# Performance work log

Hardware: AMD Instinct MI355X
Metric: run time of the kernel (lower is better)

## Reference

```python
import jax, jax.numpy as jnp
import numpy as np

B, L = 512, 8192          # batch, document length
N = 128                   # output_sentence_num
S = 256                   # output_sentence_len
DELIM = 5                 # delimiter token
PAD = 0                   # pad_word
CUT_HEAD = False
VOCAB = 100


def setup_inputs() -> dict:
    key = jax.random.key(0)
    x = jax.random.randint(key, (B, L), 0, VOCAB, dtype=jnp.int32)
    return {"x": x}


def reference(x):
    b, l = x.shape
    # right-padded row: original tokens + one trailing delimiter, shape [B, L+1]
    rpad = jnp.concatenate([x, jnp.full((b, 1), DELIM, x.dtype)], axis=1)
    # segment id of rpad position j = number of delimiters in x[:j]
    cum = jnp.cumsum((x == DELIM).astype(jnp.int32), axis=1)           # [B, L]
    seg = jnp.concatenate([jnp.zeros((b, 1), jnp.int32), cum], axis=1)  # [B, L+1]
    seg = jnp.minimum(seg, N - 1)  # segments >= N-1 merged into last chunk (tail merge)
    j = jnp.arange(l + 1, dtype=jnp.int32)
    bidx = jnp.arange(b)[:, None]
    # start index of each segment (min j with seg==k); unused segments stay at L+1
    starts = jnp.full((b, N), l + 1, jnp.int32)
    starts = starts.at[bidx, seg].min(jnp.broadcast_to(j, (b, l + 1)))
    pos = j[None, :] - jnp.take_along_axis(starts, seg, axis=1)  # offset within chunk
    # chunk sizes (number of rpad positions per segment)
    sizes = jnp.zeros((b, N), jnp.int32).at[bidx, seg].add(jnp.ones((b, l + 1), jnp.int32))
    size_here = jnp.take_along_axis(sizes, seg, axis=1)
    # size-1 chunks (lone delimiter == empty sentence) are filled with pad_word
    vals = jnp.where(size_here == 1, jnp.int32(PAD), rpad)
    if CUT_HEAD:
        p = pos - 1
        valid = (pos >= 1) & (pos <= S - 1)  # chunk[1:S], then padded to S
    else:
        p = pos
        valid = pos <= S - 1                 # chunk[:S]
    # scatter into [B, N, S]; invalid positions routed out-of-bounds and dropped
    k_idx = jnp.where(valid, seg, N)
    p_idx = jnp.where(valid, p, S)
    otp = jnp.full((b, N, S), PAD, x.dtype)
    otp = otp.at[bidx, k_idx, p_idx].set(vals, mode='drop')
    # lengths / mask (tf.count_nonzero semantics; pad_word == 0)
    len_sent = jnp.sum((otp != 0).astype(jnp.int32), axis=2)   # [B, N]
    len_doc = jnp.sum((len_sent != 0).astype(jnp.int32), axis=1)  # [B]
    mask = (jnp.arange(S)[None, None, :] < len_sent[..., None]).astype(jnp.float32)
    return otp, len_doc, mask
```

## Files before the change

### kernel.cpp

```cpp
#include <hip/hip_runtime.h>

#define B_ 512
#define L_ 8192
#define N_ 128
#define S_ 256
#define DELIM_ 5
#define T_ 1024
#define NW_ (T_ / 64)

__global__ __launch_bounds__(T_) void split_kernel(const int* __restrict__ x,
                                                   float* __restrict__ otp,
                                                   float* __restrict__ len_doc,
                                                   float* __restrict__ mask) {
    const int b = blockIdx.x;
    const int t = threadIdx.x;
    const int lane = t & 63;
    const int w = t >> 6;
    const int* __restrict__ row = x + (size_t)b * L_;

    __shared__ __align__(16) int s_row[L_ + 1];
    __shared__ int s_wsum[NW_];
    __shared__ int s_dpos[N_ - 1];
    __shared__ int s_start[N_];
    __shared__ int s_cl[N_];
    __shared__ int s_doc[NW_];

    const int4 r0 = ((const int4*)row)[t];
    const int4 r1 = ((const int4*)row)[t + T_];
    ((int4*)s_row)[t] = r0;
    ((int4*)s_row)[t + T_] = r1;
    if (t == 0) s_row[L_] = DELIM_;

    const int c0 = (r0.x == DELIM_) + (r0.y == DELIM_) + (r0.z == DELIM_) + (r0.w == DELIM_);
    const int c1 = (r1.x == DELIM_) + (r1.y == DELIM_) + (r1.z == DELIM_) + (r1.w == DELIM_);
    const int packed = c0 | (c1 << 16);

    int v = packed;
#pragma unroll
    for (int d = 1; d < 64; d <<= 1) {
        int n = __shfl_up(v, d, 64);
        if (lane >= d) v += n;
    }
    if (lane == 63) s_wsum[w] = v;
    __syncthreads();

    int woff = 0, tot = 0;
#pragma unroll
    for (int i = 0; i < NW_; ++i) {
        const int sv = s_wsum[i];
        if (i < w) woff += sv;
        tot += sv;
    }
    const int pre = woff + v - packed;
    const int c0tot = tot & 0xffff;
    const int m = c0tot + (tot >> 16);
    const int off0 = pre & 0xffff;
    const int off1 = c0tot + (pre >> 16);

    if (c0 > 0 && off0 < N_ - 1) {
        int o = off0;
        const int p = 4 * t;
        if (r0.x == DELIM_) { if (o < N_ - 1) s_dpos[o] = p;     ++o; }
        if (r0.y == DELIM_) { if (o < N_ - 1) s_dpos[o] = p + 1; ++o; }
        if (r0.z == DELIM_) { if (o < N_ - 1) s_dpos[o] = p + 2; ++o; }
        if (r0.w == DELIM_) { if (o < N_ - 1) s_dpos[o] = p + 3; ++o; }
    }
    if (c1 > 0 && off1 < N_ - 1) {
        int o = off1;
        const int p = 4 * T_ + 4 * t;
        if (r1.x == DELIM_) { if (o < N_ - 1) s_dpos[o] = p;     ++o; }
        if (r1.y == DELIM_) { if (o < N_ - 1) s_dpos[o] = p + 1; ++o; }
        if (r1.z == DELIM_) { if (o < N_ - 1) s_dpos[o] = p + 2; ++o; }
        if (r1.w == DELIM_) { if (o < N_ - 1) s_dpos[o] = p + 3; ++o; }
    }
    __syncthreads();

    if (t < N_) {
        const int k = t;
        const int mc = (m < N_ - 1) ? m : (N_ - 1);
        int start = 0, cl = 0;
        if (k <= mc) {
            start = (k == 0) ? 0 : (s_dpos[k - 1] + 1);
            const int end = (k < mc) ? s_dpos[k] : L_;
            const int size = end - start + 1;
            cl = (size <= 1) ? 0 : (size < S_ ? size : S_);
        }
        s_start[k] = start;
        s_cl[k] = cl;
    }
    __syncthreads();

    float* __restrict__ otp_b = otp + (size_t)b * N_ * S_;
    float* __restrict__ msk_b = mask + (size_t)b * N_ * S_;
    int doccnt = 0;
#pragma unroll
    for (int i = 0; i < (N_ / NW_); ++i) {
        const int k = i * NW_ + w;
        const int start = s_start[k];
        const int cl = s_cl[k];
        float tf[4];
        int len = 0;
#pragma unroll
        for (int j = 0; j < 4; ++j) {
            const int e = 64 * j + lane;
            const int tok = (e < cl) ? s_row[start + e] : 0;
            tf[j] = (float)tok;
            len += __popcll(__ballot(tok != 0));
        }
#pragma unroll
        for (int j = 0; j < 4; ++j) {
            const int e = 64 * j + lane;
            otp_b[(size_t)k * S_ + e] = tf[j];
            msk_b[(size_t)k * S_ + e] = (e < len) ? 1.0f : 0.0f;
        }
        doccnt += (len > 0);
    }

    if (lane == 0) s_doc[w] = doccnt;
    __syncthreads();
    if (t == 0) {
        int d = 0;
#pragma unroll
        for (int i = 0; i < NW_; ++i) d += s_doc[i];
        len_doc[b] = (float)d;
    }
}

extern "C" void kernel_launch(void* const* d_in, const int* in_sizes, int n_in,
                              void* d_out, int out_size, void* d_ws, size_t ws_size,
                              hipStream_t stream) {
    const int* x = (const int*)d_in[0];
    float* out = (float*)d_out;

    float* otp = out;
    float* len_doc = out + (size_t)B_ * N_ * S_;
    float* mask = len_doc + B_;

    split_kernel<<<B_, T_, 0, stream>>>(x, otp, len_doc, mask);
}
```

Before: 141.8 us.

## Split into scan kernel writing segment table and wide fill kernel

The single per-row kernel is split in two. A scan kernel computes each segment's start, clipped length and nonzero count and packs them into a workspace table. A separate fill kernel, launched over many small blocks, writes otp and mask with float4 stores, reading tokens from global memory again. The aim is to spread the large output write across more blocks and use vector stores instead of having 512 big blocks do all the writing. The cost is a second launch, a re-read of x from global memory, and a dependence on the workspace buffer.

```diff
diff --git a/kernel.cpp b/kernel.cpp
--- a/kernel.cpp
+++ b/kernel.cpp
@@ -8,10 +8,9 @@
 #define T_ 1024
 #define NW_ (T_ / 64)
 
-__global__ __launch_bounds__(T_) void split_kernel(const int* __restrict__ x,
-                                                   float* __restrict__ otp,
-                                                   float* __restrict__ len_doc,
-                                                   float* __restrict__ mask) {
+__global__ __launch_bounds__(T_) void scan_kernel(const int* __restrict__ x,
+                                                  int* __restrict__ table,
+                                                  float* __restrict__ len_doc) {
     const int b = blockIdx.x;
     const int t = threadIdx.x;
     const int lane = t & 63;
@@ -90,29 +89,20 @@
     }
     __syncthreads();
 
-    float* __restrict__ otp_b = otp + (size_t)b * N_ * S_;
-    float* __restrict__ msk_b = mask + (size_t)b * N_ * S_;
     int doccnt = 0;
 #pragma unroll
     for (int i = 0; i < (N_ / NW_); ++i) {
         const int k = i * NW_ + w;
         const int start = s_start[k];
         const int cl = s_cl[k];
-        float tf[4];
         int len = 0;
 #pragma unroll
         for (int j = 0; j < 4; ++j) {
             const int e = 64 * j + lane;
             const int tok = (e < cl) ? s_row[start + e] : 0;
-            tf[j] = (float)tok;
             len += __popcll(__ballot(tok != 0));
         }
-#pragma unroll
-        for (int j = 0; j < 4; ++j) {
-            const int e = 64 * j + lane;
-            otp_b[(size_t)k * S_ + e] = tf[j];
-            msk_b[(size_t)k * S_ + e] = (e < len) ? 1.0f : 0.0f;
-        }
+        if (lane == 0) table[b * N_ + k] = start | (cl << 14) | (len << 23);
         doccnt += (len > 0);
     }
 
@@ -126,6 +116,41 @@
     }
 }
 
+__global__ __launch_bounds__(256) void fill_kernel(const int* __restrict__ x,
+                                                   const int* __restrict__ table,
+                                                   float* __restrict__ otp,
+                                                   float* __restrict__ mask) {
+    const int g = blockIdx.x;
+    const int b = g & (B_ - 1);
+    const int strip = g >> 9;
+    const int w = threadIdx.x >> 6;
+    const int lane = threadIdx.x & 63;
+    const int k = strip * 4 + w;
+
+    const int packed = table[b * N_ + k];
+    const int start = packed & 0x3fff;
+    const int cl = (packed >> 14) & 0x1ff;
+    const int len = packed >> 23;
+
+    const int* __restrict__ row = x + (size_t)b * L_;
+    const int e0 = lane * 4;
+    float tf[4], mf[4];
+#pragma unroll
+    for (int j = 0; j < 4; ++j) {
+        const int e = e0 + j;
+        int tok = 0;
+        if (e < cl) {
+            const int gpos = start + e;
+            tok = (gpos < L_) ? row[gpos] : DELIM_;
+        }
+        tf[j] = (float)tok;
+        mf[j] = (e < len) ? 1.0f : 0.0f;
+    }
+    const size_t o = (size_t)(b * N_ + k) * S_ + e0;
+    *(float4*)(otp + o) = make_float4(tf[0], tf[1], tf[2], tf[3]);
+    *(float4*)(mask + o) = make_float4(mf[0], mf[1], mf[2], mf[3]);
+}
+
 extern "C" void kernel_launch(void* const* d_in, const int* in_sizes, int n_in,
                               void* d_out, int out_size, void* d_ws, size_t ws_size,
                               hipStream_t stream) {
@@ -136,5 +161,8 @@
     float* len_doc = out + (size_t)B_ * N_ * S_;
     float* mask = len_doc + B_;
 
-    split_kernel<<<B_, T_, 0, stream>>>(x, otp, len_doc, mask);
+    int* table = (int*)d_ws;
+
+    scan_kernel<<<B_, T_, 0, stream>>>(x, table, len_doc);
+    fill_kernel<<<(B_ * N_) / 4, 256, 0, stream>>>(x, table, otp, mask);
 }
```

Result: slower. 149.3 us (+5.3%).
